# Kernel optimization log

Measured on AMD Instinct MI355X. Metric: run time of the kernel, lower is better.

The kernel has to match this reference:

```python
import jax, jax.numpy as jnp
import numpy as np


def setup_inputs() -> dict:
    key = jax.random.key(0)
    ks = jax.random.split(key, 5)
    B = 8192
    return {
        "x": jax.random.normal(ks[0], (B, 1, 28, 28), dtype=jnp.float32),
        "conv1w": jax.random.normal(ks[1], (3, 196, 1, 2, 2), dtype=jnp.float32),
        "conv2w": jax.random.normal(ks[2], (64, 36, 3, 4, 4), dtype=jnp.float32),
        "fc1w": jax.random.normal(ks[3], (1024, 2304), dtype=jnp.float32),
        "fc2w": jax.random.normal(ks[4], (10, 1024), dtype=jnp.float32),
    }


def reference(x, conv1w, conv2w, fc1w, fc2w):
    # The torch module swaps a fresh filter into conv2d for every output pixel,
    # i.e. an unshared-weight (locally-connected) conv. Each kept pixel is
    # relu(dot(patch, per-pixel filter)), so we unfold patches and contract.
    B = x.shape[0]

    # --- layer 1: 2x2 kernel, stride 2, non-overlapping -> 14x14 = 196 pixels
    # [B,1,28,28] -> [B,14,2,14,2] -> [B,196,4] patches
    p1 = x[:, 0].reshape(B, 14, 2, 14, 2).transpose(0, 1, 3, 2, 4).reshape(B, 196, 4)
    w1 = conv1w.reshape(3, 196, 4)  # [C=3, P=196, K=4]
    out1 = jax.nn.relu(jnp.einsum('bpk,cpk->bcp', p1, w1)).reshape(B, 3, 14, 14)

    # --- layer 2: 4x4 kernel, stride 2 on 14x14 -> 6x6 = 36 pixels, 3 in-ch
    idx = 2 * jnp.arange(6)[:, None] + jnp.arange(4)[None, :]  # [6,4] row/col gather
    t = out1[:, :, idx, :]          # [B,3,6,4,14]
    t = t[:, :, :, :, idx]          # [B,3,6,4,6,4]
    # -> [B, 6, 6, 3, 4, 4] -> [B, 36, 48] (patch features in torch CHW order)
    p2 = t.transpose(0, 2, 4, 1, 3, 5).reshape(B, 36, 48)
    w2 = conv2w.reshape(64, 36, 48)  # [C=64, P=36, K=48]
    out2 = jax.nn.relu(jnp.einsum('bpk,cpk->bcp', p2, w2)).reshape(B, 2304)

    # --- fully connected head (bias-free linears)
    h = jax.nn.relu(out2 @ fc1w.T)   # [B,1024]
    return h @ fc2w.T                # [B,10]
```

## Files before the change

### kernel.cpp

```cpp
#include <hip/hip_runtime.h>
#include <hip/hip_bf16.h>

typedef __attribute__((ext_vector_type(8))) short short8;
typedef __attribute__((ext_vector_type(4))) float f32x4;
typedef __attribute__((ext_vector_type(8))) unsigned short ushort8;
typedef __attribute__((ext_vector_type(4))) unsigned short ushort4v;

__device__ __forceinline__ float bf2f(unsigned short u) {
  union { unsigned int i; float f; } v;
  v.i = ((unsigned int)u) << 16;
  return v.f;
}

__device__ __forceinline__ unsigned short f2bf(float f) {
  union { float f; unsigned int i; } v;
  v.f = f;
  unsigned int x = v.i;
  return (unsigned short)((x + 0x7FFFu + ((x >> 16) & 1u)) >> 16);
}

__device__ __forceinline__ void async_load16(const void* g, void* l) {
  __builtin_amdgcn_global_load_lds(
      (const __attribute__((address_space(1))) unsigned int*)g,
      (__attribute__((address_space(3))) unsigned int*)l, 16, 0, 0);
}

__global__ __launch_bounds__(256) void cvt_all(
    const float* __restrict__ fc1, unsigned short* __restrict__ fc1b,
    const float* __restrict__ w2, unsigned short* __restrict__ w2b) {
  __shared__ float row[2304];
  const int bx = blockIdx.x;
  const int tid = threadIdx.x;
  if (bx < 1024) {
    const float* src = fc1 + (size_t)bx * 2304;
    for (int i = tid; i < 2304; i += 256) row[i] = src[i];
    __syncthreads();
    unsigned short* dst = fc1b + (size_t)bx * 2304;
    for (int i = tid; i < 2304; i += 256) {
      int pp = i >> 6, c2 = i & 63;
      dst[i] = f2bf(row[c2 * 36 + pp]);
    }
  } else {
    const int p = bx - 1024;
    for (int i = tid; i < 3072; i += 256) {
      int c2 = i / 48, kk = i - c2 * 48;
      w2b[(size_t)p * 3072 + i] = f2bf(w2[(size_t)c2 * 1728 + p * 48 + kk]);
    }
  }
}

#define LDP 72
#define XST 260
__global__ __launch_bounds__(256) void conv_fused6(
    const float* __restrict__ x, const float* __restrict__ w1,
    const unsigned short* __restrict__ w2b, unsigned short* __restrict__ out2,
    int B) {
  __shared__ unsigned short sxb[64 * XST];
  __shared__ unsigned short s_w2[64 * LDP];
  __shared__ unsigned short s_win[64 * LDP];
  const int tid = threadIdx.x;
  const int b0 = blockIdx.x * 64;
  const int u = blockIdx.y;

  {
    int bi = tid >> 2, q = tid & 3;
    ushort4v z = {0, 0, 0, 0};
    *(ushort4v*)&s_win[bi * LDP + 48 + 4 * q] = z;
    *(ushort4v*)&s_w2[bi * LDP + 48 + 4 * q] = z;
  }

  for (int i = tid; i < 3584; i += 256) {
    int bi = i / 56, rem = i - bi * 56;
    int r = rem / 7, c7 = rem - r * 7;
    float4 v = *(const float4*)(x + (size_t)(b0 + bi) * 784 +
                                (4 * u + r) * 28 + c7 * 4);
    ushort4v o;
    o[0] = f2bf(v.x); o[1] = f2bf(v.y); o[2] = f2bf(v.z); o[3] = f2bf(v.w);
    *(ushort4v*)&sxb[bi * XST + r * 32 + c7 * 4] = o;
  }

  const int lane = tid & 63, wave = tid >> 6;
  const int wm = wave >> 1, wn = wave & 1;
  const int fr = lane & 15, fo = (lane >> 4) * 8;

  for (int u2 = 0; u2 < 6; ++u2) {
    const int p = u * 6 + u2;
    __syncthreads();

    {
      const unsigned short* src = w2b + (size_t)p * 3072;
      for (int i = tid; i < 384; i += 256) {
        int c2 = i / 6, q = i - c2 * 6;
        *(ushort8*)&s_w2[c2 * LDP + q * 8] = *(const ushort8*)(src + i * 8);
      }
    }

    for (int it = tid; it < 768; it += 256) {
      int bi = it & 63, cv = it >> 6;
      int c = cv >> 2, v = cv & 3;
      const unsigned short* r0p = &sxb[bi * XST + (2 * v) * 32 + 4 * u2];
      ushort4v a0 = *(const ushort4v*)r0p;
      ushort4v a1 = *(const ushort4v*)(r0p + 4);
      ushort4v b0v = *(const ushort4v*)(r0p + 32);
      ushort4v b1v = *(const ushort4v*)(r0p + 36);
      const float* wbase = w1 + ((c * 196 + (2 * u + v) * 14 + 2 * u2) << 2);
      float4 q0 = *(const float4*)(wbase);
      float4 q1 = *(const float4*)(wbase + 4);
      float4 q2 = *(const float4*)(wbase + 8);
      float4 q3 = *(const float4*)(wbase + 12);
      ushort4v o;
      o[0] = f2bf(fmaxf(bf2f(a0[0]) * q0.x + bf2f(a0[1]) * q0.y +
                        bf2f(b0v[0]) * q0.z + bf2f(b0v[1]) * q0.w, 0.f));
      o[1] = f2bf(fmaxf(bf2f(a0[2]) * q1.x + bf2f(a0[3]) * q1.y +
                        bf2f(b0v[2]) * q1.z + bf2f(b0v[3]) * q1.w, 0.f));
      o[2] = f2bf(fmaxf(bf2f(a1[0]) * q2.x + bf2f(a1[1]) * q2.y +
                        bf2f(b1v[0]) * q2.z + bf2f(b1v[1]) * q2.w, 0.f));
      o[3] = f2bf(fmaxf(bf2f(a1[2]) * q3.x + bf2f(a1[3]) * q3.y +
                        bf2f(b1v[2]) * q3.z + bf2f(b1v[3]) * q3.w, 0.f));
      *(ushort4v*)&s_win[bi * LDP + 4 * cv] = o;
    }
    __syncthreads();

    f32x4 acc[2][2] = {};
    #pragma unroll
    for (int k2 = 0; k2 < 2; ++k2) {
      short8 af[2], bf[2];
      #pragma unroll
      for (int m = 0; m < 2; ++m)
        af[m] = *(const short8*)&s_win[(wm * 32 + m * 16 + fr) * LDP + k2 * 32 + fo];
      #pragma unroll
      for (int n = 0; n < 2; ++n)
        bf[n] = *(const short8*)&s_w2[(wn * 32 + n * 16 + fr) * LDP + k2 * 32 + fo];
      #pragma unroll
      for (int m = 0; m < 2; ++m)
        #pragma unroll
        for (int n = 0; n < 2; ++n)
          acc[m][n] = __builtin_amdgcn_mfma_f32_16x16x32_bf16(af[m], bf[n],
                                                              acc[m][n], 0, 0, 0);
    }
    __syncthreads();

    unsigned short* s_out = s_win;
    const int r0 = wm * 32 + (lane >> 4) * 4;
    const int c0 = wn * 32 + fr;
    #pragma unroll
    for (int m = 0; m < 2; ++m)
      #pragma unroll
      for (int n = 0; n < 2; ++n)
        #pragma unroll
        for (int j = 0; j < 4; ++j)
          s_out[(r0 + m * 16 + j) * 64 + (c0 + n * 16)] =
              f2bf(fmaxf(acc[m][n][j], 0.f));
    __syncthreads();

    for (int it = tid; it < 512; it += 256) {
      int row = it >> 3, ch = it & 7;
      *(short8*)(out2 + (size_t)(b0 + row) * 2304 + p * 64 + ch * 8) =
          *(const short8*)&s_out[row * 64 + ch * 8];
    }
  }
}

#define GBM 128
#define GBN 128
#define GBK 64

__global__ __launch_bounds__(512) void gemm_fc1_fc2(
    const unsigned short* __restrict__ A,
    const unsigned short* __restrict__ Bw,
    const float* __restrict__ Wfc2,
    float* __restrict__ out,
    int K, int NT) {
  __shared__ unsigned short sA[2 * GBM * GBK];
  __shared__ unsigned short sB[2 * GBN * GBK];
  __shared__ float sW[10 * GBN];
  const int tid = threadIdx.x;
  const int lane = tid & 63;
  const int wave = tid >> 6;
  const int wm = wave >> 2, wn = wave & 3;
  const size_t m0 = (size_t)blockIdx.x * GBM;
  const size_t n0 = (size_t)blockIdx.y * GBN;

  const int r8 = tid >> 3;
  const int c8 = tid & 7;
  const int ksw = (c8 ^ (r8 & 7)) * 8;
  const unsigned short* Ag = A + (m0 + r8) * (size_t)K + ksw;
  const unsigned short* Bg = Bw + (n0 + r8) * (size_t)K + ksw;
  unsigned short* sAp = &sA[r8 * GBK + c8 * 8];
  unsigned short* sBp = &sB[r8 * GBK + c8 * 8];

#define STAGE_A(buf, t, i) \
  async_load16(Ag + (size_t)(t) * GBK + (size_t)(i) * 64 * K, \
               sAp + (buf) * (GBM * GBK) + (i) * 64 * GBK)
#define STAGE_B(buf, t, i) \
  async_load16(Bg + (size_t)(t) * GBK + (size_t)(i) * 64 * K, \
               sBp + (buf) * (GBN * GBK) + (i) * 64 * GBK)
#define STAGE_TILE(buf, t) \
  STAGE_A(buf, t, 0); STAGE_A(buf, t, 1); STAGE_B(buf, t, 0); STAGE_B(buf, t, 1)

  STAGE_TILE(0, 0);

  const int fr = lane & 15, fg = lane >> 4, fx = lane & 7;
  int aBase[4], bBase[2];
  #pragma unroll
  for (int m = 0; m < 4; ++m) aBase[m] = (wm * 64 + m * 16 + fr) * GBK;
  #pragma unroll
  for (int n = 0; n < 2; ++n) bBase[n] = (wn * 32 + n * 16 + fr) * GBK;
  const int jc0 = (fg ^ fx) * 8;
  const int jc1 = jc0 ^ 32;

  f32x4 acc[4][2] = {};

  for (int t = 0; t < NT; ++t) {
    const int cur = t & 1;
    if (t + 1 < NT) {
      STAGE_TILE(cur ^ 1, t + 1);
      asm volatile("s_waitcnt vmcnt(4)" ::: "memory");
    } else {
      asm volatile("s_waitcnt vmcnt(0)" ::: "memory");
    }
    __builtin_amdgcn_s_barrier();

    const unsigned short* As = &sA[cur * GBM * GBK];
    const unsigned short* Bs = &sB[cur * GBN * GBK];
    short8 a0[4], a1[4], b0[2], b1[2];
    #pragma unroll
    for (int m = 0; m < 4; ++m) {
      a0[m] = *(const short8*)&As[aBase[m] + jc0];
      a1[m] = *(const short8*)&As[aBase[m] + jc1];
    }
    #pragma unroll
    for (int n = 0; n < 2; ++n) {
      b0[n] = *(const short8*)&Bs[bBase[n] + jc0];
      b1[n] = *(const short8*)&Bs[bBase[n] + jc1];
    }
    __builtin_amdgcn_s_setprio(1);
    #pragma unroll
    for (int m = 0; m < 4; ++m)
      #pragma unroll
      for (int n = 0; n < 2; ++n)
        acc[m][n] = __builtin_amdgcn_mfma_f32_16x16x32_bf16(a0[m], b0[n],
                                                            acc[m][n], 0, 0, 0);
    #pragma unroll
    for (int m = 0; m < 4; ++m)
      #pragma unroll
      for (int n = 0; n < 2; ++n)
        acc[m][n] = __builtin_amdgcn_mfma_f32_16x16x32_bf16(a1[m], b1[n],
                                                            acc[m][n], 0, 0, 0);
    __builtin_amdgcn_s_setprio(0);
    __builtin_amdgcn_s_barrier();
  }

  for (int i = tid; i < 10 * GBN; i += 512)
    sW[i] = Wfc2[(i >> 7) * 1024 + n0 + (i & 127)];

  unsigned short* hs = sA;
  #pragma unroll
  for (int m = 0; m < 4; ++m)
    #pragma unroll
    for (int n = 0; n < 2; ++n)
      #pragma unroll
      for (int j = 0; j < 4; ++j) {
        int row = wm * 64 + m * 16 + fg * 4 + j;
        int col = wn * 32 + n * 16 + fr;
        hs[row * 128 + (col ^ ((row & 7) << 3))] =
            f2bf(fmaxf(acc[m][n][j], 0.f));
      }
  __syncthreads();

  {
    const int row = tid >> 2;
    const int quar = tid & 3;
    const int r7s = (row & 7) << 3;
    float hv[32];
    #pragma unroll
    for (int c = 0; c < 4; ++c) {
      int base = quar * 32 + c * 8;
      short8 u = *(const short8*)&hs[row * 128 + (base ^ r7s)];
      #pragma unroll
      for (int q = 0; q < 8; ++q) hv[c * 8 + q] = bf2f((unsigned short)u[q]);
    }
    float* op = out + (m0 + row) * 10;
    #pragma unroll
    for (int o = 0; o < 10; ++o) {
      const float* wr = &sW[o * 128 + quar * 32];
      float a = 0.f;
      #pragma unroll
      for (int q = 0; q < 32; ++q) a += hv[q] * wr[q];
      a += __shfl_down(a, 1);
      a += __shfl_down(a, 2);
      if (quar == 0) atomicAdd(&op[o], a);
    }
  }
#undef STAGE_A
#undef STAGE_B
#undef STAGE_TILE
}

extern "C" void kernel_launch(void* const* d_in, const int* in_sizes, int n_in,
                              void* d_out, int out_size, void* d_ws, size_t ws_size,
                              hipStream_t stream) {
  const float* x   = (const float*)d_in[0];
  const float* w1  = (const float*)d_in[1];
  const float* w2  = (const float*)d_in[2];
  const float* fc1 = (const float*)d_in[3];
  const float* fc2 = (const float*)d_in[4];
  float* out = (float*)d_out;
  const int B = in_sizes[0] / 784;

  unsigned short* out2 = (unsigned short*)d_ws;
  unsigned short* fc1b = out2 + (size_t)B * 2304;
  unsigned short* w2b  = fc1b + (size_t)1024 * 2304;

  hipMemsetAsync(out, 0, (size_t)out_size * sizeof(float), stream);
  cvt_all<<<1060, 256, 0, stream>>>(fc1, fc1b, w2, w2b);
  dim3 cg(B / 64, 6);
  conv_fused6<<<cg, 256, 0, stream>>>(x, w1, w2b, out2, B);
  dim3 g(B / GBM, 1024 / GBN);
  gemm_fc1_fc2<<<g, 512, 0, stream>>>(out2, fc1b, fc2, out, 2304, 2304 / GBK);
}
```

Baseline: 101.0 us.

## Merge weight conversion into conv kernel and split K across waves in FC GEMM

Removes the separate conversion kernel. The fc1 transpose-convert now runs as extra blocks of the conv kernel, and conv2 weights are converted from fp32 inside each conv block as they are loaded. The conv1 stage now computes eight outputs per thread instead of four. In the fc1 GEMM, each wave now covers a 64x64 output tile over half of each K step, and the two K halves are summed through shared memory before the fused fc2 epilogue, which cuts LDS fragment loads per MFMA. The costs are redundant conv2 weight conversion in every conv block, an extra shared-memory reduction with barriers, more accumulator registers, and a grid size hard-coded to the batch of 8192.

```diff
diff --git a/kernel.cpp b/kernel.cpp
--- a/kernel.cpp
+++ b/kernel.cpp
@@ -25,48 +25,39 @@
       (__attribute__((address_space(3))) unsigned int*)l, 16, 0, 0);
 }
 
-__global__ __launch_bounds__(256) void cvt_all(
-    const float* __restrict__ fc1, unsigned short* __restrict__ fc1b,
-    const float* __restrict__ w2, unsigned short* __restrict__ w2b) {
-  __shared__ float row[2304];
-  const int bx = blockIdx.x;
-  const int tid = threadIdx.x;
-  if (bx < 1024) {
-    const float* src = fc1 + (size_t)bx * 2304;
-    for (int i = tid; i < 2304; i += 256) row[i] = src[i];
-    __syncthreads();
-    unsigned short* dst = fc1b + (size_t)bx * 2304;
-    for (int i = tid; i < 2304; i += 256) {
-      int pp = i >> 6, c2 = i & 63;
-      dst[i] = f2bf(row[c2 * 36 + pp]);
-    }
-  } else {
-    const int p = bx - 1024;
-    for (int i = tid; i < 3072; i += 256) {
-      int c2 = i / 48, kk = i - c2 * 48;
-      w2b[(size_t)p * 3072 + i] = f2bf(w2[(size_t)c2 * 1728 + p * 48 + kk]);
-    }
-  }
-}
-
 #define LDP 72
 #define XST 260
-__global__ __launch_bounds__(256) void conv_fused6(
+__global__ __launch_bounds__(256) void conv_cvt(
     const float* __restrict__ x, const float* __restrict__ w1,
-    const unsigned short* __restrict__ w2b, unsigned short* __restrict__ out2,
-    int B) {
+    const float* __restrict__ w2, unsigned short* __restrict__ out2,
+    const float* __restrict__ fc1, unsigned short* __restrict__ fc1b, int B) {
   __shared__ unsigned short sxb[64 * XST];
   __shared__ unsigned short s_w2[64 * LDP];
   __shared__ unsigned short s_win[64 * LDP];
   const int tid = threadIdx.x;
-  const int b0 = blockIdx.x * 64;
-  const int u = blockIdx.y;
+  const int bid = blockIdx.x;
+
+  if (bid >= 768) {
+    float* rowbuf = (float*)sxb;
+    const int n = bid - 768;
+    const float* src = fc1 + (size_t)n * 2304;
+    for (int i = tid; i < 2304; i += 256) rowbuf[i] = src[i];
+    __syncthreads();
+    unsigned short* dst = fc1b + (size_t)n * 2304;
+    for (int i = tid; i < 2304; i += 256) {
+      int pp = i >> 6, c2 = i & 63;
+      dst[i] = f2bf(rowbuf[c2 * 36 + pp]);
+    }
+    return;
+  }
+
+  const int b0 = (bid & 127) * 64;
+  const int u = bid >> 7;
 
   {
     int bi = tid >> 2, q = tid & 3;
     ushort4v z = {0, 0, 0, 0};
     *(ushort4v*)&s_win[bi * LDP + 48 + 4 * q] = z;
-    *(ushort4v*)&s_w2[bi * LDP + 48 + 4 * q] = z;
   }
 
   for (int i = tid; i < 3584; i += 256) {
@@ -88,36 +79,53 @@
     __syncthreads();
 
     {
-      const unsigned short* src = w2b + (size_t)p * 3072;
-      for (int i = tid; i < 384; i += 256) {
-        int c2 = i / 6, q = i - c2 * 6;
-        *(ushort8*)&s_w2[c2 * LDP + q * 8] = *(const ushort8*)(src + i * 8);
+      const float* w2p = w2 + (size_t)p * 48;
+      for (int i = tid; i < 4096; i += 256) {
+        int c2 = i >> 6, kk = i & 63;
+        float v = (kk < 48) ? w2p[(size_t)c2 * 1728 + kk] : 0.f;
+        s_w2[c2 * LDP + kk] = f2bf(v);
       }
     }
 
-    for (int it = tid; it < 768; it += 256) {
-      int bi = it & 63, cv = it >> 6;
-      int c = cv >> 2, v = cv & 3;
-      const unsigned short* r0p = &sxb[bi * XST + (2 * v) * 32 + 4 * u2];
-      ushort4v a0 = *(const ushort4v*)r0p;
-      ushort4v a1 = *(const ushort4v*)(r0p + 4);
-      ushort4v b0v = *(const ushort4v*)(r0p + 32);
-      ushort4v b1v = *(const ushort4v*)(r0p + 36);
-      const float* wbase = w1 + ((c * 196 + (2 * u + v) * 14 + 2 * u2) << 2);
-      float4 q0 = *(const float4*)(wbase);
-      float4 q1 = *(const float4*)(wbase + 4);
-      float4 q2 = *(const float4*)(wbase + 8);
-      float4 q3 = *(const float4*)(wbase + 12);
-      ushort4v o;
-      o[0] = f2bf(fmaxf(bf2f(a0[0]) * q0.x + bf2f(a0[1]) * q0.y +
-                        bf2f(b0v[0]) * q0.z + bf2f(b0v[1]) * q0.w, 0.f));
-      o[1] = f2bf(fmaxf(bf2f(a0[2]) * q1.x + bf2f(a0[3]) * q1.y +
-                        bf2f(b0v[2]) * q1.z + bf2f(b0v[3]) * q1.w, 0.f));
-      o[2] = f2bf(fmaxf(bf2f(a1[0]) * q2.x + bf2f(a1[1]) * q2.y +
-                        bf2f(b1v[0]) * q2.z + bf2f(b1v[1]) * q2.w, 0.f));
-      o[3] = f2bf(fmaxf(bf2f(a1[2]) * q3.x + bf2f(a1[3]) * q3.y +
-                        bf2f(b1v[2]) * q3.z + bf2f(b1v[3]) * q3.w, 0.f));
-      *(ushort4v*)&s_win[bi * LDP + 4 * cv] = o;
+    for (int it = tid; it < 384; it += 256) {
+      int bi = it & 63, c8 = it >> 6;
+      int c = c8 >> 1, v0 = (c8 & 1) * 2;
+      const unsigned short* xr = &sxb[bi * XST + 2 * v0 * 32 + 4 * u2];
+      ushort4v r0a = *(const ushort4v*)(xr);
+      ushort4v r0b = *(const ushort4v*)(xr + 4);
+      ushort4v r1a = *(const ushort4v*)(xr + 32);
+      ushort4v r1b = *(const ushort4v*)(xr + 36);
+      ushort4v r2a = *(const ushort4v*)(xr + 64);
+      ushort4v r2b = *(const ushort4v*)(xr + 68);
+      ushort4v r3a = *(const ushort4v*)(xr + 96);
+      ushort4v r3b = *(const ushort4v*)(xr + 100);
+      const float* wb0 = w1 + ((c * 196 + (2 * u + v0) * 14 + 2 * u2) << 2);
+      float4 q0 = *(const float4*)(wb0);
+      float4 q1 = *(const float4*)(wb0 + 4);
+      float4 q2 = *(const float4*)(wb0 + 8);
+      float4 q3 = *(const float4*)(wb0 + 12);
+      float4 q4 = *(const float4*)(wb0 + 56);
+      float4 q5 = *(const float4*)(wb0 + 60);
+      float4 q6 = *(const float4*)(wb0 + 64);
+      float4 q7 = *(const float4*)(wb0 + 68);
+      ushort8 o;
+      o[0] = f2bf(fmaxf(bf2f(r0a[0]) * q0.x + bf2f(r0a[1]) * q0.y +
+                        bf2f(r1a[0]) * q0.z + bf2f(r1a[1]) * q0.w, 0.f));
+      o[1] = f2bf(fmaxf(bf2f(r0a[2]) * q1.x + bf2f(r0a[3]) * q1.y +
+                        bf2f(r1a[2]) * q1.z + bf2f(r1a[3]) * q1.w, 0.f));
+      o[2] = f2bf(fmaxf(bf2f(r0b[0]) * q2.x + bf2f(r0b[1]) * q2.y +
+                        bf2f(r1b[0]) * q2.z + bf2f(r1b[1]) * q2.w, 0.f));
+      o[3] = f2bf(fmaxf(bf2f(r0b[2]) * q3.x + bf2f(r0b[3]) * q3.y +
+                        bf2f(r1b[2]) * q3.z + bf2f(r1b[3]) * q3.w, 0.f));
+      o[4] = f2bf(fmaxf(bf2f(r2a[0]) * q4.x + bf2f(r2a[1]) * q4.y +
+                        bf2f(r3a[0]) * q4.z + bf2f(r3a[1]) * q4.w, 0.f));
+      o[5] = f2bf(fmaxf(bf2f(r2a[2]) * q5.x + bf2f(r2a[3]) * q5.y +
+                        bf2f(r3a[2]) * q5.z + bf2f(r3a[3]) * q5.w, 0.f));
+      o[6] = f2bf(fmaxf(bf2f(r2b[0]) * q6.x + bf2f(r2b[1]) * q6.y +
+                        bf2f(r3b[0]) * q6.z + bf2f(r3b[1]) * q6.w, 0.f));
+      o[7] = f2bf(fmaxf(bf2f(r2b[2]) * q7.x + bf2f(r2b[3]) * q7.y +
+                        bf2f(r3b[2]) * q7.z + bf2f(r3b[3]) * q7.w, 0.f));
+      *(ushort8*)&s_win[bi * LDP + c8 * 8] = o;
     }
     __syncthreads();
 
@@ -158,6 +166,12 @@
       *(short8*)(out2 + (size_t)(b0 + row) * 2304 + p * 64 + ch * 8) =
           *(const short8*)&s_out[row * 64 + ch * 8];
     }
+    __syncthreads();
+    {
+      int bi = tid >> 2, q = tid & 3;
+      ushort4v z = {0, 0, 0, 0};
+      *(ushort4v*)&s_win[bi * LDP + 48 + 4 * q] = z;
+    }
   }
 }
 
@@ -165,19 +179,20 @@
 #define GBN 128
 #define GBK 64
 
-__global__ __launch_bounds__(512) void gemm_fc1_fc2(
+__global__ __launch_bounds__(512, 4) void gemm_fc1_fc2(
     const unsigned short* __restrict__ A,
     const unsigned short* __restrict__ Bw,
     const float* __restrict__ Wfc2,
     float* __restrict__ out,
     int K, int NT) {
-  __shared__ unsigned short sA[2 * GBM * GBK];
-  __shared__ unsigned short sB[2 * GBN * GBK];
+  __shared__ unsigned short smem[2 * (GBM + GBN) * GBK];
   __shared__ float sW[10 * GBN];
+  unsigned short* sA = smem;
+  unsigned short* sB = smem + 2 * GBM * GBK;
   const int tid = threadIdx.x;
   const int lane = tid & 63;
   const int wave = tid >> 6;
-  const int wm = wave >> 2, wn = wave & 3;
+  const int kz = wave & 1, wn = (wave >> 1) & 1, wm = wave >> 2;
   const size_t m0 = (size_t)blockIdx.x * GBM;
   const size_t n0 = (size_t)blockIdx.y * GBN;
 
@@ -201,15 +216,14 @@
   STAGE_TILE(0, 0);
 
   const int fr = lane & 15, fg = lane >> 4, fx = lane & 7;
-  int aBase[4], bBase[2];
+  const int jck = ((fg ^ fx) * 8) ^ (kz << 5);
+  int aBase[4], bBase[4];
   #pragma unroll
-  for (int m = 0; m < 4; ++m) aBase[m] = (wm * 64 + m * 16 + fr) * GBK;
+  for (int m = 0; m < 4; ++m) aBase[m] = (wm * 64 + m * 16 + fr) * GBK + jck;
   #pragma unroll
-  for (int n = 0; n < 2; ++n) bBase[n] = (wn * 32 + n * 16 + fr) * GBK;
-  const int jc0 = (fg ^ fx) * 8;
-  const int jc1 = jc0 ^ 32;
-
-  f32x4 acc[4][2] = {};
+  for (int n = 0; n < 4; ++n) bBase[n] = (wn * 64 + n * 16 + fr) * GBK + jck;
+
+  f32x4 acc[4][4] = {};
 
   for (int t = 0; t < NT; ++t) {
     const int cur = t & 1;
@@ -223,49 +237,69 @@
 
     const unsigned short* As = &sA[cur * GBM * GBK];
     const unsigned short* Bs = &sB[cur * GBN * GBK];
-    short8 a0[4], a1[4], b0[2], b1[2];
-    #pragma unroll
-    for (int m = 0; m < 4; ++m) {
-      a0[m] = *(const short8*)&As[aBase[m] + jc0];
-      a1[m] = *(const short8*)&As[aBase[m] + jc1];
-    }
-    #pragma unroll
-    for (int n = 0; n < 2; ++n) {
-      b0[n] = *(const short8*)&Bs[bBase[n] + jc0];
-      b1[n] = *(const short8*)&Bs[bBase[n] + jc1];
-    }
+    short8 af[4], bf[4];
+    #pragma unroll
+    for (int m = 0; m < 4; ++m) af[m] = *(const short8*)&As[aBase[m]];
+    #pragma unroll
+    for (int n = 0; n < 4; ++n) bf[n] = *(const short8*)&Bs[bBase[n]];
     __builtin_amdgcn_s_setprio(1);
     #pragma unroll
     for (int m = 0; m < 4; ++m)
       #pragma unroll
-      for (int n = 0; n < 2; ++n)
-        acc[m][n] = __builtin_amdgcn_mfma_f32_16x16x32_bf16(a0[m], b0[n],
-                                                            acc[m][n], 0, 0, 0);
-    #pragma unroll
-    for (int m = 0; m < 4; ++m)
-      #pragma unroll
-      for (int n = 0; n < 2; ++n)
-        acc[m][n] = __builtin_amdgcn_mfma_f32_16x16x32_bf16(a1[m], b1[n],
+      for (int n = 0; n < 4; ++n)
+        acc[m][n] = __builtin_amdgcn_mfma_f32_16x16x32_bf16(af[m], bf[n],
                                                             acc[m][n], 0, 0, 0);
     __builtin_amdgcn_s_setprio(0);
     __builtin_amdgcn_s_barrier();
   }
+  __syncthreads();
 
   for (int i = tid; i < 10 * GBN; i += 512)
     sW[i] = Wfc2[(i >> 7) * 1024 + n0 + (i & 127)];
 
-  unsigned short* hs = sA;
-  #pragma unroll
-  for (int m = 0; m < 4; ++m)
-    #pragma unroll
-    for (int n = 0; n < 2; ++n)
-      #pragma unroll
-      for (int j = 0; j < 4; ++j) {
-        int row = wm * 64 + m * 16 + fg * 4 + j;
-        int col = wn * 32 + n * 16 + fr;
-        hs[row * 128 + (col ^ ((row & 7) << 3))] =
-            f2bf(fmaxf(acc[m][n][j], 0.f));
-      }
+  float* fs = (float*)smem;
+  const int reg = (wm * 2 + wn) * 4096;
+  if (kz == 1) {
+    #pragma unroll
+    for (int m = 0; m < 4; ++m)
+      #pragma unroll
+      for (int n = 0; n < 4; ++n)
+        #pragma unroll
+        for (int j = 0; j < 4; ++j) {
+          int row = m * 16 + fg * 4 + j;
+          int col = (n * 16 + fr) ^ (fg << 4);
+          fs[reg + row * 64 + col] = acc[m][n][j];
+        }
+  }
+  __syncthreads();
+  if (kz == 0) {
+    #pragma unroll
+    for (int m = 0; m < 4; ++m)
+      #pragma unroll
+      for (int n = 0; n < 4; ++n)
+        #pragma unroll
+        for (int j = 0; j < 4; ++j) {
+          int row = m * 16 + fg * 4 + j;
+          int col = (n * 16 + fr) ^ (fg << 4);
+          acc[m][n][j] += fs[reg + row * 64 + col];
+        }
+  }
+  __syncthreads();
+
+  unsigned short* hs = smem;
+  if (kz == 0) {
+    #pragma unroll
+    for (int m = 0; m < 4; ++m)
+      #pragma unroll
+      for (int n = 0; n < 4; ++n)
+        #pragma unroll
+        for (int j = 0; j < 4; ++j) {
+          int row = wm * 64 + m * 16 + fg * 4 + j;
+          int col = wn * 64 + n * 16 + fr;
+          hs[row * 128 + (col ^ ((row & 7) << 3))] =
+              f2bf(fmaxf(acc[m][n][j], 0.f));
+        }
+  }
   __syncthreads();
 
   {
@@ -310,12 +344,9 @@
 
   unsigned short* out2 = (unsigned short*)d_ws;
   unsigned short* fc1b = out2 + (size_t)B * 2304;
-  unsigned short* w2b  = fc1b + (size_t)1024 * 2304;
 
   hipMemsetAsync(out, 0, (size_t)out_size * sizeof(float), stream);
-  cvt_all<<<1060, 256, 0, stream>>>(fc1, fc1b, w2, w2b);
-  dim3 cg(B / 64, 6);
-  conv_fused6<<<cg, 256, 0, stream>>>(x, w1, w2b, out2, B);
+  conv_cvt<<<768 + 1024, 256, 0, stream>>>(x, w1, w2, out2, fc1, fc1b, B);
   dim3 g(B / GBM, 1024 / GBN);
   gemm_fc1_fc2<<<g, 512, 0, stream>>>(out2, fc1b, fc2, out, 2304, 2304 / GBK);
 }
```

After: 118.9 us. 17.7% more time.

## Enlarge FC1 GEMM tile to 256x128 with triple-buffered interleaved prefetch

Applied to the files above, without the earlier changes.

The fused FC1+FC2 GEMM tile grows from 128x128 to 256x128, so each of the 8 waves now computes a 64x64 sub-tile. Global-to-LDS staging moves from a double buffer to a triple buffer that prefetches two tiles ahead. Each K-tile is split into four phases, and each phase interleaves LDS fragment reads, part of the async prefetch, and an MFMA burst. The aim is more reuse per LDS byte and better overlap of memory traffic with matrix math. The cost is more accumulator registers, more LDS (three stages of A and B), and half as many blocks, which may reduce occupancy and grid fill.

```diff
diff --git a/kernel.cpp b/kernel.cpp
--- a/kernel.cpp
+++ b/kernel.cpp
@@ -161,23 +161,24 @@
   }
 }
 
-#define GBM 128
+#define GBM 256
 #define GBN 128
 #define GBK 64
-
-__global__ __launch_bounds__(512) void gemm_fc1_fc2(
+#define ASZ (GBM * GBK)
+#define BSZ (GBN * GBK)
+
+__global__ __launch_bounds__(512) void gemm8p(
     const unsigned short* __restrict__ A,
     const unsigned short* __restrict__ Bw,
     const float* __restrict__ Wfc2,
     float* __restrict__ out,
     int K, int NT) {
-  __shared__ unsigned short sA[2 * GBM * GBK];
-  __shared__ unsigned short sB[2 * GBN * GBK];
+  __shared__ unsigned short smem[3 * (ASZ + BSZ)];
   __shared__ float sW[10 * GBN];
   const int tid = threadIdx.x;
   const int lane = tid & 63;
   const int wave = tid >> 6;
-  const int wm = wave >> 2, wn = wave & 3;
+  const int wm = wave >> 1, wn = wave & 1;
   const size_t m0 = (size_t)blockIdx.x * GBM;
   const size_t n0 = (size_t)blockIdx.y * GBN;
 
@@ -186,96 +187,143 @@
   const int ksw = (c8 ^ (r8 & 7)) * 8;
   const unsigned short* Ag = A + (m0 + r8) * (size_t)K + ksw;
   const unsigned short* Bg = Bw + (n0 + r8) * (size_t)K + ksw;
-  unsigned short* sAp = &sA[r8 * GBK + c8 * 8];
-  unsigned short* sBp = &sB[r8 * GBK + c8 * 8];
-
-#define STAGE_A(buf, t, i) \
+  const int dst = r8 * GBK + c8 * 8;
+
+#define STG_A(buf, t, i) \
   async_load16(Ag + (size_t)(t) * GBK + (size_t)(i) * 64 * K, \
-               sAp + (buf) * (GBM * GBK) + (i) * 64 * GBK)
-#define STAGE_B(buf, t, i) \
+               smem + (buf) * ASZ + (i) * 4096 + dst)
+#define STG_B(buf, t, i) \
   async_load16(Bg + (size_t)(t) * GBK + (size_t)(i) * 64 * K, \
-               sBp + (buf) * (GBN * GBK) + (i) * 64 * GBK)
-#define STAGE_TILE(buf, t) \
-  STAGE_A(buf, t, 0); STAGE_A(buf, t, 1); STAGE_B(buf, t, 0); STAGE_B(buf, t, 1)
-
-  STAGE_TILE(0, 0);
+               smem + 3 * ASZ + (buf) * BSZ + (i) * 4096 + dst)
+
+  STG_A(0, 0, 0); STG_A(0, 0, 1); STG_A(0, 0, 2); STG_A(0, 0, 3);
+  STG_B(0, 0, 0); STG_B(0, 0, 1);
+  STG_A(1, 1, 0); STG_A(1, 1, 1); STG_A(1, 1, 2); STG_A(1, 1, 3);
+  STG_B(1, 1, 0); STG_B(1, 1, 1);
 
   const int fr = lane & 15, fg = lane >> 4, fx = lane & 7;
-  int aBase[4], bBase[2];
+  const int jc0 = (fg ^ fx) * 8;
+  int aOff[4], bOff[4];
   #pragma unroll
-  for (int m = 0; m < 4; ++m) aBase[m] = (wm * 64 + m * 16 + fr) * GBK;
+  for (int m = 0; m < 4; ++m) aOff[m] = (wm * 64 + m * 16 + fr) * GBK + jc0;
   #pragma unroll
-  for (int n = 0; n < 2; ++n) bBase[n] = (wn * 32 + n * 16 + fr) * GBK;
-  const int jc0 = (fg ^ fx) * 8;
-  const int jc1 = jc0 ^ 32;
-
-  f32x4 acc[4][2] = {};
+  for (int n = 0; n < 4; ++n) bOff[n] = (wn * 64 + n * 16 + fr) * GBK + jc0;
+
+  asm volatile("s_waitcnt vmcnt(6)" ::: "memory");
+  __builtin_amdgcn_s_barrier();
+
+  f32x4 acc[4][4] = {};
 
   for (int t = 0; t < NT; ++t) {
-    const int cur = t & 1;
+    const int cb = t - (t / 3) * 3;
+    const unsigned short* As = smem + cb * ASZ;
+    const unsigned short* Bs = smem + 3 * ASZ + cb * BSZ;
+    const int t2 = t + 2;
+    const int sb = t2 - (t2 / 3) * 3;
+    const bool st = t2 < NT;
+    short8 af[4], bq[2];
+
+    #pragma unroll
+    for (int m = 0; m < 4; ++m) af[m] = *(const short8*)&As[aOff[m]];
+    bq[0] = *(const short8*)&Bs[bOff[0]];
+    bq[1] = *(const short8*)&Bs[bOff[1]];
+    if (st) { STG_A(sb, t2, 0); STG_A(sb, t2, 1); }
+    __builtin_amdgcn_s_barrier();
+    asm volatile("s_waitcnt lgkmcnt(0)" ::: "memory");
+    __builtin_amdgcn_s_setprio(1);
+    #pragma unroll
+    for (int m = 0; m < 4; ++m)
+      acc[m][0] = __builtin_amdgcn_mfma_f32_16x16x32_bf16(af[m], bq[0], acc[m][0], 0, 0, 0);
+    #pragma unroll
+    for (int m = 0; m < 4; ++m)
+      acc[m][1] = __builtin_amdgcn_mfma_f32_16x16x32_bf16(af[m], bq[1], acc[m][1], 0, 0, 0);
+    __builtin_amdgcn_s_setprio(0);
+    __builtin_amdgcn_s_barrier();
+
+    #pragma unroll
+    for (int m = 0; m < 4; ++m) af[m] = *(const short8*)&As[aOff[m]];
+    bq[0] = *(const short8*)&Bs[bOff[2]];
+    bq[1] = *(const short8*)&Bs[bOff[3]];
+    if (st) { STG_A(sb, t2, 2); STG_A(sb, t2, 3); }
+    __builtin_amdgcn_s_barrier();
+    asm volatile("s_waitcnt lgkmcnt(0)" ::: "memory");
+    __builtin_amdgcn_s_setprio(1);
+    #pragma unroll
+    for (int m = 0; m < 4; ++m)
+      acc[m][2] = __builtin_amdgcn_mfma_f32_16x16x32_bf16(af[m], bq[0], acc[m][2], 0, 0, 0);
+    #pragma unroll
+    for (int m = 0; m < 4; ++m)
+      acc[m][3] = __builtin_amdgcn_mfma_f32_16x16x32_bf16(af[m], bq[1], acc[m][3], 0, 0, 0);
+    __builtin_amdgcn_s_setprio(0);
+    __builtin_amdgcn_s_barrier();
+
+    #pragma unroll
+    for (int m = 0; m < 4; ++m) af[m] = *(const short8*)&As[aOff[m] ^ 32];
+    bq[0] = *(const short8*)&Bs[bOff[0] ^ 32];
+    bq[1] = *(const short8*)&Bs[bOff[1] ^ 32];
+    if (st) { STG_B(sb, t2, 0); STG_B(sb, t2, 1); }
+    __builtin_amdgcn_s_barrier();
+    asm volatile("s_waitcnt lgkmcnt(0)" ::: "memory");
+    __builtin_amdgcn_s_setprio(1);
+    #pragma unroll
+    for (int m = 0; m < 4; ++m)
+      acc[m][0] = __builtin_amdgcn_mfma_f32_16x16x32_bf16(af[m], bq[0], acc[m][0], 0, 0, 0);
+    #pragma unroll
+    for (int m = 0; m < 4; ++m)
+      acc[m][1] = __builtin_amdgcn_mfma_f32_16x16x32_bf16(af[m], bq[1], acc[m][1], 0, 0, 0);
+    __builtin_amdgcn_s_setprio(0);
+    __builtin_amdgcn_s_barrier();
+
+    #pragma unroll
+    for (int m = 0; m < 4; ++m) af[m] = *(const short8*)&As[aOff[m] ^ 32];
+    bq[0] = *(const short8*)&Bs[bOff[2] ^ 32];
+    bq[1] = *(const short8*)&Bs[bOff[3] ^ 32];
+    __builtin_amdgcn_s_barrier();
+    asm volatile("s_waitcnt lgkmcnt(0)" ::: "memory");
+    __builtin_amdgcn_s_setprio(1);
+    #pragma unroll
+    for (int m = 0; m < 4; ++m)
+      acc[m][2] = __builtin_amdgcn_mfma_f32_16x16x32_bf16(af[m], bq[0], acc[m][2], 0, 0, 0);
+    #pragma unroll
+    for (int m = 0; m < 4; ++m)
+      acc[m][3] = __builtin_amdgcn_mfma_f32_16x16x32_bf16(af[m], bq[1], acc[m][3], 0, 0, 0);
+    __builtin_amdgcn_s_setprio(0);
     if (t + 1 < NT) {
-      STAGE_TILE(cur ^ 1, t + 1);
-      asm volatile("s_waitcnt vmcnt(4)" ::: "memory");
-    } else {
-      asm volatile("s_waitcnt vmcnt(0)" ::: "memory");
-    }
-    __builtin_amdgcn_s_barrier();
-
-    const unsigned short* As = &sA[cur * GBM * GBK];
-    const unsigned short* Bs = &sB[cur * GBN * GBK];
-    short8 a0[4], a1[4], b0[2], b1[2];
-    #pragma unroll
-    for (int m = 0; m < 4; ++m) {
-      a0[m] = *(const short8*)&As[aBase[m] + jc0];
-      a1[m] = *(const short8*)&As[aBase[m] + jc1];
-    }
-    #pragma unroll
-    for (int n = 0; n < 2; ++n) {
-      b0[n] = *(const short8*)&Bs[bBase[n] + jc0];
-      b1[n] = *(const short8*)&Bs[bBase[n] + jc1];
-    }
-    __builtin_amdgcn_s_setprio(1);
-    #pragma unroll
-    for (int m = 0; m < 4; ++m)
-      #pragma unroll
-      for (int n = 0; n < 2; ++n)
-        acc[m][n] = __builtin_amdgcn_mfma_f32_16x16x32_bf16(a0[m], b0[n],
-                                                            acc[m][n], 0, 0, 0);
-    #pragma unroll
-    for (int m = 0; m < 4; ++m)
-      #pragma unroll
-      for (int n = 0; n < 2; ++n)
-        acc[m][n] = __builtin_amdgcn_mfma_f32_16x16x32_bf16(a1[m], b1[n],
-                                                            acc[m][n], 0, 0, 0);
-    __builtin_amdgcn_s_setprio(0);
-    __builtin_amdgcn_s_barrier();
-  }
+      if (t + 1 == NT - 1) {
+        asm volatile("s_waitcnt vmcnt(0)" ::: "memory");
+      } else {
+        asm volatile("s_waitcnt vmcnt(6)" ::: "memory");
+      }
+    }
+    __builtin_amdgcn_s_barrier();
+  }
+  __syncthreads();
 
   for (int i = tid; i < 10 * GBN; i += 512)
     sW[i] = Wfc2[(i >> 7) * 1024 + n0 + (i & 127)];
 
-  unsigned short* hs = sA;
+  unsigned short* hs = smem;
   #pragma unroll
   for (int m = 0; m < 4; ++m)
     #pragma unroll
-    for (int n = 0; n < 2; ++n)
+    for (int n = 0; n < 4; ++n)
       #pragma unroll
       for (int j = 0; j < 4; ++j) {
         int row = wm * 64 + m * 16 + fg * 4 + j;
-        int col = wn * 32 + n * 16 + fr;
+        int col = wn * 64 + n * 16 + fr;
         hs[row * 128 + (col ^ ((row & 7) << 3))] =
             f2bf(fmaxf(acc[m][n][j], 0.f));
       }
   __syncthreads();
 
   {
-    const int row = tid >> 2;
-    const int quar = tid & 3;
+    const int row = tid >> 1;
+    const int half = tid & 1;
     const int r7s = (row & 7) << 3;
-    float hv[32];
-    #pragma unroll
-    for (int c = 0; c < 4; ++c) {
-      int base = quar * 32 + c * 8;
+    float hv[64];
+    #pragma unroll
+    for (int c = 0; c < 8; ++c) {
+      int base = half * 64 + c * 8;
       short8 u = *(const short8*)&hs[row * 128 + (base ^ r7s)];
       #pragma unroll
       for (int q = 0; q < 8; ++q) hv[c * 8 + q] = bf2f((unsigned short)u[q]);
@@ -283,18 +331,16 @@
     float* op = out + (m0 + row) * 10;
     #pragma unroll
     for (int o = 0; o < 10; ++o) {
-      const float* wr = &sW[o * 128 + quar * 32];
+      const float* wr = &sW[o * 128 + half * 64];
       float a = 0.f;
       #pragma unroll
-      for (int q = 0; q < 32; ++q) a += hv[q] * wr[q];
+      for (int q = 0; q < 64; ++q) a += hv[q] * wr[q];
       a += __shfl_down(a, 1);
-      a += __shfl_down(a, 2);
-      if (quar == 0) atomicAdd(&op[o], a);
-    }
-  }
-#undef STAGE_A
-#undef STAGE_B
-#undef STAGE_TILE
+      if (half == 0) atomicAdd(&op[o], a);
+    }
+  }
+#undef STG_A
+#undef STG_B
 }
 
 extern "C" void kernel_launch(void* const* d_in, const int* in_sizes, int n_in,
@@ -317,5 +363,5 @@
   dim3 cg(B / 64, 6);
   conv_fused6<<<cg, 256, 0, stream>>>(x, w1, w2b, out2, B);
   dim3 g(B / GBM, 1024 / GBN);
-  gemm_fc1_fc2<<<g, 512, 0, stream>>>(out2, fc1b, fc2, out, 2304, 2304 / GBK);
-}
+  gemm8p<<<g, 512, 0, stream>>>(out2, fc1b, fc2, out, 2304, 2304 / GBK);
+}
```

New measurement: 116.9 us. 1.16x slower.
